# Kernel tuning notes

Measured on AMD Instinct MI355X. Metric: run time of the kernel, lower is better.

The kernel has to match this reference:

```python
import jax, jax.numpy as jnp
import numpy as np

NUM_CLASSES = 80
TOPK = 1000
CONF_THRESH = 0.05
NMS_THRESH = 0.6
IMG = 1280.0  # input image H = W
LEVEL_N = [230400, 57600, 14400, 3600, 900]  # (1280/stride)^2 * 9 anchors, strides 8..128


def _make_boxes(k, n):
    kc, kw = jax.random.split(k)
    cxcy = jax.random.uniform(kc, (n, 2), jnp.float32, 0.0, IMG)
    wh = jax.random.uniform(kw, (n, 2), jnp.float32, 8.0, 256.0)
    x1y1 = jnp.clip(cxcy - 0.5 * wh, 0.0, IMG)
    x2y2 = jnp.clip(cxcy + 0.5 * wh, 0.0, IMG)
    return jnp.concatenate([x1y1, x2y2], axis=-1)  # [n,4] xyxy pixel coords


def setup_inputs() -> dict:
    key = jax.random.key(0)
    keys = jax.random.split(key, 10)
    inp = {}
    for i, n in enumerate(LEVEL_N):
        inp[f"cls{i}"] = jax.random.normal(keys[i], (n, NUM_CLASSES), jnp.float32) - 2.0
        inp[f"box{i}"] = _make_boxes(keys[5 + i], n)
    return inp


def _level_topk(cls_l, box_l):
    # cls_l: [N, C] logits, box_l: [N, 4]
    n = cls_l.shape[0]
    scores = jax.nn.sigmoid(cls_l).reshape(-1)           # [N*C]
    k = min(TOPK, n)
    top_scores, top_idx = jax.lax.top_k(scores, k)       # fused sort/topk per level
    labels = top_idx % NUM_CLASSES
    anchor = top_idx // NUM_CLASSES
    boxes = box_l[anchor]                                # irregular gather
    valid = top_scores > CONF_THRESH
    return top_scores, labels, boxes, valid


def _pairwise_iou(b):
    # b: [M,4] xyxy
    area = jnp.maximum(b[:, 2] - b[:, 0], 0.0) * jnp.maximum(b[:, 3] - b[:, 1], 0.0)
    lt = jnp.maximum(b[:, None, :2], b[None, :, :2])
    rb = jnp.minimum(b[:, None, 2:], b[None, :, 2:])
    wh = jnp.maximum(rb - lt, 0.0)
    inter = wh[..., 0] * wh[..., 1]
    return inter / (area[:, None] + area[None, :] - inter + 1e-9)


def _greedy_nms(boxes, scores, labels, valid):
    # class-aware greedy NMS via per-class coordinate offset trick
    m = scores.shape[0]
    s = jnp.where(valid, scores, 0.0)
    order = jnp.argsort(-s)
    boxes = boxes[order]
    s = s[order]
    labels = labels[order]
    valid = valid[order]
    offset = labels.astype(boxes.dtype)[:, None] * (IMG + 1.0)
    ious = _pairwise_iou(boxes + offset)                 # [M,M]
    idx = jnp.arange(m)

    def body(i, keep):
        sup = keep[i] & (ious[i] > NMS_THRESH) & (idx > i)
        return keep & ~sup

    keep = jax.lax.fori_loop(0, m, body, valid)
    return boxes, s, labels, keep


def reference(cls0, cls1, cls2, cls3, cls4, box0, box1, box2, box3, box4):
    cls_preds = [cls0, cls1, cls2, cls3, cls4]
    box_preds = [box0, box1, box2, box3, box4]
    parts = [_level_topk(c, b) for c, b in zip(cls_preds, box_preds)]
    scores = jnp.concatenate([p[0] for p in parts])
    labels = jnp.concatenate([p[1] for p in parts])
    boxes = jnp.concatenate([p[2] for p in parts])
    valid = jnp.concatenate([p[3] for p in parts])
    boxes, scores, labels, keep = _greedy_nms(boxes, scores, labels, valid)
    keepf = keep.astype(boxes.dtype)
    bboxes = jnp.clip(boxes / IMG, 0.0, 1.0) * keepf[:, None]  # normalize like inference_single_image
    scores = scores * keepf
    return bboxes, scores, labels, keep
```

## Files before the change

kernel.cpp:

```cpp
#include <hip/hip_runtime.h>
#include <cmath>

typedef unsigned int u32;
typedef unsigned long long u64;

#define NLEV 5
#define M_TOT 4900
#define NWORDS 77
#define CSTRIDE 80
#define PAD_M 4928
#define NBLK 1501
#define LDSQ 2048
#define NSH 32
#define SHCAP 2048
#define OVCAP 16384
#define LVST (NSH*SHCAP + OVCAP)
#define TIE_CAP 2048
#define NBLK_CMAT 3003
#define HBINS 4096
#define UCAP 128

__constant__ int   c_KLVL[5] = {1000,1000,1000,1000,900};
__constant__ int   c_LOFF[5] = {0,1000,2000,3000,4000};
__constant__ int   c_N4[5]   = {4608000,1152000,288000,72000,18000};
__constant__ int   c_BB[6]   = {0,1125,1407,1478,1496,1501};
__constant__ float c_THR[5]  = {1.0f,0.65f,0.30f,-0.15f,-0.60f};

constexpr size_t OFF_CNT   = 0;
constexpr size_t OFF_OCNT  = 768;
constexpr size_t OFF_KEPT  = 1024;
constexpr size_t OFF_HPRED = 2048;
constexpr size_t ZERO_BYTES= 4096;
constexpr size_t OFF_CAND  = 4096;
constexpr size_t OFF_KEY   = OFF_CAND + (size_t)NLEV*LVST*8;
constexpr size_t OFF_RAWB  = OFF_KEY   + (size_t)PAD_M*8;
constexpr size_t OFF_OFFB  = OFF_RAWB  + (size_t)PAD_M*16;
constexpr size_t OFF_LAB   = OFF_OFFB  + (size_t)PAD_M*16;
constexpr size_t OFF_SVAL  = OFF_LAB   + (size_t)PAD_M*4;
constexpr size_t OFF_VALID = OFF_SVAL  + (size_t)PAD_M*4;
constexpr size_t OFF_SRAWB = OFF_VALID + (size_t)PAD_M*4;
constexpr size_t OFF_SOFFB = OFF_SRAWB + (size_t)PAD_M*16;
constexpr size_t OFF_SLAB  = OFF_SOFFB + (size_t)PAD_M*16;
constexpr size_t OFF_SSVAL = OFF_SLAB  + (size_t)PAD_M*4;
constexpr size_t OFF_SVALID= OFF_SSVAL + (size_t)PAD_M*4;
constexpr size_t OFF_CMAT  = (OFF_SVALID + (size_t)PAD_M*4 + 255) & ~(size_t)255;

__device__ __forceinline__ u32 okey(u32 u){
  return (u & 0x80000000u) ? ~u : (u | 0x80000000u);
}

__device__ __forceinline__ u32 qbin(u32 bits, float T){
  float x = __uint_as_float(bits);
  int b = (int)((x - T)*800.0f);
  return (u32)max(0, min(HBINS-1, b));
}

__device__ __forceinline__ u32 lane_prior(u64 mask){
  return __builtin_amdgcn_mbcnt_hi((u32)(mask>>32),
         __builtin_amdgcn_mbcnt_lo((u32)mask, 0u));
}

__device__ __forceinline__ u32 wave_alloc(u32* ctr, bool take){
  u64 mask = __ballot(take);
  if (mask==0ull) return 0xFFFFFFFFu;
  u32 prior = lane_prior(mask);
  u32 total = (u32)__popcll(mask);
  int leader = __ffsll((unsigned long long)mask) - 1;
  u32 base = 0;
  if (take && prior==0u) base = atomicAdd(ctr, total);
  base = __shfl(base, leader, 64);
  return take ? (base + prior) : 0xFFFFFFFFu;
}

__global__ void __launch_bounds__(256)
k_collect(const float* __restrict__ a0, const float* __restrict__ a1,
          const float* __restrict__ a2, const float* __restrict__ a3,
          const float* __restrict__ a4,
          u32* __restrict__ cnt, u32* __restrict__ ocnt, u32* __restrict__ cand)
{
  const int b = blockIdx.x;
  const int l = (b<c_BB[1])?0:(b<c_BB[2])?1:(b<c_BB[3])?2:(b<c_BB[4])?3:4;
  const float* __restrict__ p = (l==0)?a0:(l==1)?a1:(l==2)?a2:(l==3)?a3:a4;
  const float T = c_THR[l];
  const int n4l = c_N4[l];
  const int lb  = b - c_BB[l];
  const int shard = lb & (NSH-1);
  const int base4 = lb*4096 + (int)threadIdx.x;

  __shared__ u32 lcnt, gbase;
  __shared__ u32 lbitsA[LDSQ];
  __shared__ u32 lidxA[LDSQ];
  if (threadIdx.x==0) lcnt=0u;
  __syncthreads();

  float4 xs[16];
#pragma unroll
  for (int u=0;u<16;u++){
    int q = base4 + u*256;
    int qc = (q < n4l) ? q : (n4l-1);
    xs[u] = *(const float4*)(p + (size_t)qc*4u);
  }
  u32* cdS = cand + ((size_t)l*LVST + (size_t)shard*SHCAP)*2u;
  u32* cdO = cand + ((size_t)l*LVST + (size_t)NSH*SHCAP)*2u;
#pragma unroll
  for (int u=0;u<16;u++){
    int q = base4 + u*256;
    if (q < n4l){
      float v[4]={xs[u].x,xs[u].y,xs[u].z,xs[u].w};
#pragma unroll
      for (int i=0;i<4;i++){
        if (v[i] > T){
          u32 s = atomicAdd(&lcnt,1u);
          u32 bits = __float_as_uint(v[i]);
          u32 idx  = (u32)(q*4+i);
          if (s < LDSQ){ lbitsA[s]=bits; lidxA[s]=idx; }
          else {
            u32 pp = atomicAdd(&ocnt[l],1u);
            if (pp < OVCAP){ u32* d=cdO+(size_t)pp*2u; d[0]=bits; d[1]=idx; }
          }
        }
      }
    }
  }
  __syncthreads();
  if (threadIdx.x==0){
    u32 m = min(lcnt,(u32)LDSQ);
    gbase = (m>0u) ? atomicAdd(&cnt[l*NSH+shard],m) : 0xFFFFFFFFu;
  }
  __syncthreads();
  u32 m = min(lcnt,(u32)LDSQ);
  for (u32 i=threadIdx.x;i<m;i+=256u){
    u32 pp = gbase + i;
    if (pp < SHCAP){ u32* d=cdS+(size_t)pp*2u; d[0]=lbitsA[i]; d[1]=lidxA[i]; }
    else {
      u32 q = atomicAdd(&ocnt[l],1u);
      if (q < OVCAP){ u32* d=cdO+(size_t)q*2u; d[0]=lbitsA[i]; d[1]=lidxA[i]; }
    }
  }
}

__device__ __forceinline__ void emit_record(int l, int slot, u32 lbits, u32 idx,
    const float4* __restrict__ boxp, u64* keyA, float4* rawbA, float4* offbA,
    u32* labA, float* svalA, u32* validA)
{
#pragma clang fp contract(off)
  float x = __uint_as_float(lbits);
  float s = (float)(1.0 / (1.0 + exp(-(double)x)));
  u32 valid = (s > 0.05f) ? 1u : 0u;
  u32 label = idx % 80u;
  u32 anchor = idx / 80u;
  float4 bx = boxp[anchor];
  float off = (float)label * 1281.0f;
  float4 ob;
  ob.x = bx.x + off; ob.y = bx.y + off; ob.z = bx.z + off; ob.w = bx.w + off;
  u32 pos = ((u32)l << 25) | idx;
  u32 khi = valid ? okey(lbits) : 0u;
  int g = c_LOFF[l] + slot;
  keyA[g]  = ((u64)khi << 32) | (u64)(u32)(~pos);
  rawbA[g] = bx; offbA[g] = ob; labA[g] = label;
  svalA[g] = valid ? s : 0.0f; validA[g] = valid;
}

__device__ __forceinline__ void emit_dummy(int l, int slot,
    u64* keyA, float4* rawbA, float4* offbA, u32* labA, float* svalA, u32* validA)
{
  u32 pos = ((u32)l<<25) | (0x1FFFFFFu - (u32)slot);
  int g = c_LOFF[l]+slot;
  float4 z; z.x=z.y=z.z=z.w=0.0f;
  keyA[g]=(u64)(u32)(~pos);
  rawbA[g]=z; offbA[g]=z; labA[g]=0u; svalA[g]=0.0f; validA[g]=0u;
}

__global__ void __launch_bounds__(1024)
k_select(u32* __restrict__ cnt, u32* __restrict__ ocnt, u32* __restrict__ cand,
         const float* __restrict__ a0, const float* __restrict__ a1,
         const float* __restrict__ a2, const float* __restrict__ a3,
         const float* __restrict__ a4,
         const float4* b0, const float4* b1, const float4* b2,
         const float4* b3, const float4* b4,
         u64* keyA, float4* rawbA, float4* offbA,
         u32* labA, float* svalA, u32* validA)
{
  const int l = blockIdx.x;
  const float4* boxp = (l==0)?b0:(l==1)?b1:(l==2)?b2:(l==3)?b3:b4;
  const float* __restrict__ p = (l==0)?a0:(l==1)?a1:(l==2)?a2:(l==3)?a3:a4;
  const float Tl = c_THR[l];
  u32* lvbase = cand + (size_t)l*LVST*2u;
  u32* cdO = lvbase + (size_t)NSH*SHCAP*2u;
  const int k = c_KLVL[l];

  __shared__ u32 lhist[4][HBINS];
  __shared__ u32 sufw[16];
  __shared__ u32 rlen[NSH+1];
  __shared__ u32 count_s;
  __shared__ u32 c0_s, kk_s;
  __shared__ u32 emit_s, ntie_s;
  __shared__ u32 tb[TIE_CAP], ti[TIE_CAP];

  const u32 tid = threadIdx.x;
  const u32 lane = tid & 63u;
  const u32 wave = tid >> 6;
  if (tid==0){ emit_s=0u; ntie_s=0u; c0_s=0u; kk_s=0u; }
  if (tid<NSH) rlen[tid]=min(cnt[l*NSH+tid],(u32)SHCAP);
  if (tid==NSH) rlen[NSH]=min(ocnt[l],(u32)OVCAP);
  for (u32 i=tid;i<4u*HBINS;i+=1024u) ((u32*)lhist)[i]=0u;
  __syncthreads();
  if (tid==0){ u32 c=0; for(int r=0;r<=NSH;r++) c+=rlen[r]; count_s=c; }
  __syncthreads();
  u32 count = count_s;

  if (count < (u32)k){
    const int nElem = c_N4[l]*4;
    float Tprev = Tl;
    for (int r=1; r<=7 && count<(u32)k; r++){
      float Tn = (r<7) ? (Tl - 1.5f*(float)r) : -3.0e38f;
      for (u32 i=tid; i<(u32)nElem; i+=1024u){
        float x = p[i];
        if (x>Tn && x<=Tprev){
          u32 pp = atomicAdd(&ocnt[l],1u);
          if (pp<OVCAP){ u32* d=cdO+(size_t)pp*2u; d[0]=__float_as_uint(x); d[1]=i; }
        }
      }
      __syncthreads();
      if (tid==0){
        rlen[NSH]=min(atomicAdd(&ocnt[l],0u),(u32)OVCAP);
        u32 c=0; for(int rr=0;rr<=NSH;rr++) c+=rlen[rr]; count_s=c;
      }
      __syncthreads();
      count = count_s;
      Tprev = Tn;
    }
  }

  if (count > (u32)k){
    const u32 rep = wave & 3u;
    for (int r=0;r<=NSH;r++){
      const u32* cdR = lvbase + ((r<NSH)?(size_t)r*SHCAP:(size_t)NSH*SHCAP)*2u;
      u32 len = rlen[r];
      for (u32 i=tid;i<len;i+=1024u)
        atomicAdd(&lhist[rep][qbin(cdR[2*(size_t)i],Tl)], 1u);
    }
    __syncthreads();
    u32 base = tid*4u;
    u32 hb[4]; u32 ls=0u;
#pragma unroll
    for (int b2_=0;b2_<4;b2_++){
      u32 h = lhist[0][base+(u32)b2_]+lhist[1][base+(u32)b2_]
            + lhist[2][base+(u32)b2_]+lhist[3][base+(u32)b2_];
      hb[b2_]=h; ls+=h;
    }
    u32 x = ls;
#pragma unroll
    for (int off=1; off<64; off<<=1){
      u32 y = __shfl_down(x, off, 64);
      if (lane + (u32)off < 64u) x += y;
    }
    if (lane==0u) sufw[wave]=x;
    __syncthreads();
    u32 wsuf=0u;
    for (u32 w=wave+1u;w<16u;w++) wsuf += sufw[w];
    u32 suffix_after = wsuf + (x - ls);
    if (suffix_after < (u32)k && (u32)k <= suffix_after + ls){
      u32 run = suffix_after;
      for (int b2_=3;b2_>=0;b2_--){
        u32 h = hb[b2_];
        run += h;
        if (run >= (u32)k){ c0_s = base+(u32)b2_; kk_s = (u32)k - (run - h); break; }
      }
    }
    __syncthreads();
    const u32 c0 = c0_s, kk = kk_s;

    for (int r=0;r<=NSH;r++){
      const u32* cdR = lvbase + ((r<NSH)?(size_t)r*SHCAP:(size_t)NSH*SHCAP)*2u;
      u32 len = rlen[r];
      u32 iters = (len + 1023u)/1024u;
      for (u32 it=0; it<iters; it++){
        u32 i = it*1024u + tid;
        bool in = i < len;
        u32 bits = in ? cdR[2*(size_t)i] : 0u;
        u32 idx  = in ? cdR[2*(size_t)i+1] : 0u;
        u32 h    = qbin(bits,Tl);
        bool hi  = in && (h > c0);
        bool tie = in && (h == c0);
        u32 s = wave_alloc(&emit_s, hi);
        if (hi && s < (u32)k)
          emit_record(l,(int)s,bits,idx,boxp,keyA,rawbA,offbA,labA,svalA,validA);
        u32 t = wave_alloc(&ntie_s, tie);
        if (tie && t < (u32)TIE_CAP){ tb[t]=bits; ti[t]=idx; }
      }
    }
    __syncthreads();

    u32 nt = ntie_s;
    if (nt <= (u32)TIE_CAP){
      for (u32 e=tid;e<nt;e+=1024u){
        u32 mk = okey(tb[e]); u32 mi = ti[e];
        u32 r=0u;
        for (u32 e2=0;e2<nt;e2++){
          u32 k2 = okey(tb[e2]);
          r += (k2>mk || (k2==mk && ti[e2]<mi)) ? 1u : 0u;
        }
        if (r < kk){
          u32 s = atomicAdd(&emit_s,1u);
          if (s < (u32)k)
            emit_record(l,(int)s,tb[e],mi,boxp,keyA,rawbA,offbA,labA,svalA,validA);
        }
      }
    } else {
      for (int r=0;r<=NSH;r++){
        const u32* cdR = lvbase + ((r<NSH)?(size_t)r*SHCAP:(size_t)NSH*SHCAP)*2u;
        u32 len = rlen[r];
        for (u32 i=tid;i<len;i+=1024u){
          u32 bits=cdR[2*(size_t)i], idx=cdR[2*(size_t)i+1];
          if (qbin(bits,Tl)!=c0) continue;
          u32 mk=okey(bits); u32 rank=0u;
          for (int r2=0;r2<=NSH;r2++){
            const u32* c2 = lvbase + ((r2<NSH)?(size_t)r2*SHCAP:(size_t)NSH*SHCAP)*2u;
            u32 len2 = rlen[r2];
            for (u32 j=0;j<len2;j++){
              u32 b2=c2[2*(size_t)j];
              if (qbin(b2,Tl)!=c0) continue;
              u32 k2=okey(b2);
              rank += (k2>mk || (k2==mk && c2[2*(size_t)j+1]<idx)) ? 1u : 0u;
            }
          }
          if (rank<kk){
            u32 s=atomicAdd(&emit_s,1u);
            if (s<(u32)k)
              emit_record(l,(int)s,bits,idx,boxp,keyA,rawbA,offbA,labA,svalA,validA);
          }
        }
      }
    }
  } else {
    for (int r=0;r<=NSH;r++){
      const u32* cdR = lvbase + ((r<NSH)?(size_t)r*SHCAP:(size_t)NSH*SHCAP)*2u;
      u32 len = rlen[r];
      u32 iters = (len + 1023u)/1024u;
      for (u32 it=0; it<iters; it++){
        u32 i = it*1024u + tid;
        bool in = i < len;
        u32 bits = in ? cdR[2*(size_t)i] : 0u;
        u32 idx  = in ? cdR[2*(size_t)i+1] : 0u;
        u32 s = wave_alloc(&emit_s, in);
        if (in && s < (u32)k)
          emit_record(l,(int)s,bits,idx,boxp,keyA,rawbA,offbA,labA,svalA,validA);
      }
    }
  }
  __syncthreads();
  u32 em = min(emit_s,(u32)k);
  for (u32 i=em+tid;i<(u32)k;i+=1024u)
    emit_dummy(l,(int)i,keyA,rawbA,offbA,labA,svalA,validA);
}

__global__ void __launch_bounds__(256)
k_rank(const u64* __restrict__ keyA,
       const float4* __restrict__ rawbA, const float4* __restrict__ offbA,
       const u32* __restrict__ labA, const float* __restrict__ svalA,
       const u32* __restrict__ validA,
       float4* srawb, float4* soffb, u32* slab, float* ssval, u32* svalid)
{
  __shared__ u64 sk[M_TOT];
  __shared__ u32 part[3][64];
  for (int i=threadIdx.x;i<M_TOT;i+=256) sk[i]=keyA[i];
  __syncthreads();
  int lane = threadIdx.x & 63;
  int wave = threadIdx.x >> 6;
  int i = blockIdx.x*64 + lane;
  u64 mk = sk[(i<M_TOT)?i:0];
  int j0 = wave*1225;
  u32 r=0;
#pragma unroll 5
  for (int j=j0;j<j0+1225;j++) r += (sk[j]>mk)?1u:0u;
  if (wave) part[wave-1][lane]=r;
  __syncthreads();
  if (wave==0 && i<M_TOT){
    r += part[0][lane]+part[1][lane]+part[2][lane];
    srawb[r]=rawbA[i]; soffb[r]=offbA[i]; slab[r]=labA[i];
    ssval[r]=svalA[i]; svalid[r]=validA[i];
  }
}

__global__ void __launch_bounds__(256)
k_cmat(const float4* __restrict__ soffb, u64* __restrict__ cmat,
       u64* __restrict__ haspred)
{
#pragma clang fp contract(off)
  int bi = blockIdx.x;
  int jt = (int)((sqrtf(8.0f*(float)bi+1.0f)-1.0f)*0.5f);
  while ((jt+1)*(jt+2)/2 <= bi) jt++;
  while (jt*(jt+1)/2 > bi) jt--;
  int wt = bi - jt*(jt+1)/2;

  __shared__ float rx[64],ry[64],rz[64],rw[64],ra[64];
  __shared__ float cx[64],cy[64],cz[64],cw[64],cae[64];
  int tid = threadIdx.x;
  if (tid<64){
    float4 b = soffb[wt*64+tid];
    rx[tid]=b.x; ry[tid]=b.y; rz[tid]=b.z; rw[tid]=b.w;
    ra[tid]=fmaxf(b.z-b.x,0.0f)*fmaxf(b.w-b.y,0.0f);
  } else if (tid<128){
    int c=tid-64;
    float4 b = soffb[jt*64+c];
    cx[c]=b.x; cy[c]=b.y; cz[c]=b.z; cw[c]=b.w;
    cae[c]=fmaxf(b.z-b.x,0.0f)*fmaxf(b.w-b.y,0.0f);
  }
  __syncthreads();
  int lane = tid & 63;
  int wave = tid >> 6;
  int rowg = wt*64 + lane;
  float bx=rx[lane], by=ry[lane], bz=rz[lane], bw=rw[lane], bar=ra[lane];
  for (int cc=wave*16; cc<wave*16+16; cc++){
    int jg = jt*64 + cc;
    if (jg >= M_TOT) continue;
    float jx=cx[cc], jy=cy[cc], jz=cz[cc], jw=cw[cc], jar=cae[cc];
    float ltx=fmaxf(bx,jx), lty=fmaxf(by,jy);
    float rbx=fminf(bz,jz), rby=fminf(bw,jw);
    float wx=fmaxf(rbx-ltx,0.0f), wy=fmaxf(rby-lty,0.0f);
    float inter=wx*wy;
    float iou = inter/(bar+jar-inter+1e-9f);
    bool bit = (rowg < jg) && (iou > 0.6f);
    u64 word = __ballot(bit);
    if (lane==0){
      cmat[(size_t)jg*CSTRIDE + (size_t)wt] = word;
      if (word) atomicOr(&haspred[jg>>6], 1ull<<(jg&63));
    }
  }
}

__global__ void __launch_bounds__(256)
k_resolve(const u64* __restrict__ cmat, const u32* __restrict__ svalid,
          const u64* __restrict__ haspred, u64* __restrict__ kept)
{
  __shared__ u64 k0[NWORDS];
  __shared__ u64 uw[NWORDS];
  __shared__ u32 ubase[NWORDS];
  __shared__ unsigned short ulist[UCAP];
  __shared__ u64 pmask[UCAP][2];
  __shared__ u32 dhit[UCAP];
  __shared__ u32 nu_s;
  const u32 tid=threadIdx.x, lane=tid&63u, wave=tid>>6;

  for (u32 w=wave; w<NWORDS; w+=4){
    int j = (int)(w*64u+lane);
    u32 sv = (j<M_TOT)? svalid[j] : 0u;
    u64 hp = haspred[w];
    bool hpb = (hp>>lane)&1ull;
    u64 keepb = __ballot(sv && !hpb);
    u64 undb  = __ballot(sv && hpb);
    if (lane==0){ k0[w]=keepb; uw[w]=undb; }
  }
  __syncthreads();
  if (tid==0){
    u32 n=0;
    for (int w=0;w<NWORDS;w++){
      ubase[w]=n;
      u64 U=uw[w];
      while(U){ int b=__builtin_ctzll(U); U&=U-1ull;
                if (n<UCAP) ulist[n]=(unsigned short)(w*64+b); n++; }
    }
    nu_s=n;
  }
  __syncthreads();
  u32 nu = nu_s;

  if (nu>0u && nu<=UCAP){
    for (u32 t=tid; t<nu; t+=256u){
      u32 j = (u32)ulist[t];
      const u64* row = cmat + (size_t)j*CSTRIDE;
      u32 wmax = j>>6;
      u64 hit=0ull, pm0=0ull, pm1=0ull;
      for (u32 w=0; w<=wmax; w++){
        u64 rw = row[w];
        hit |= rw & k0[w];
        u64 ub = rw & uw[w];
        while(ub){
          int b=__builtin_ctzll(ub); ub&=ub-1ull;
          u32 idx = ubase[w] + (u32)__popcll(uw[w] & ((b==0)?0ull:((1ull<<b)-1ull)));
          if (idx<64u) pm0 |= 1ull<<idx; else pm1 |= 1ull<<(idx-64u);
        }
      }
      dhit[t] = (hit!=0ull)?1u:0u;
      pmask[t][0]=pm0; pmask[t][1]=pm1;
    }
    __syncthreads();
    if (tid==0){
      u64 ku0=0ull, ku1=0ull;
      for (u32 t=0;t<nu;t++){
        bool sup = dhit[t] || ((pmask[t][0]&ku0)|(pmask[t][1]&ku1))!=0ull;
        if (!sup){
          if (t<64u) ku0|=1ull<<t; else ku1|=1ull<<(t-64u);
          u32 j=(u32)ulist[t];
          k0[j>>6] |= 1ull<<(j&63u);
        }
      }
    }
    __syncthreads();
  } else if (nu>UCAP){
    if (tid==0){
      for (int w=0;w<NWORDS;w++){
        u64 U=uw[w];
        while(U){
          int b=__builtin_ctzll(U); U&=U-1ull;
          u32 j=(u32)(w*64+b);
          const u64* row = cmat + (size_t)j*CSTRIDE;
          u64 hit=0ull; u32 wmax=j>>6;
          for (u32 w2=0;w2<=wmax;w2++) hit |= row[w2] & k0[w2];
          if (hit==0ull) k0[j>>6] |= 1ull<<(j&63u);
        }
      }
    }
    __syncthreads();
  }
  for (u32 w=tid; w<NWORDS; w+=256u) kept[w]=k0[w];
}

__global__ void k_out(const u64* __restrict__ kept, const float4* __restrict__ srawb,
                      const float* __restrict__ ssval, const u32* __restrict__ slab,
                      float* __restrict__ out)
{
  int t=blockIdx.x*blockDim.x+threadIdx.x;
  if (t<M_TOT){
    u32 kb=(u32)((kept[t>>6]>>(t&63))&1ull);
    float kf=kb?1.0f:0.0f;
    float4 b=srawb[t];
    out[4*t+0]=fminf(fmaxf(b.x/1280.0f,0.0f),1.0f)*kf;
    out[4*t+1]=fminf(fmaxf(b.y/1280.0f,0.0f),1.0f)*kf;
    out[4*t+2]=fminf(fmaxf(b.z/1280.0f,0.0f),1.0f)*kf;
    out[4*t+3]=fminf(fmaxf(b.w/1280.0f,0.0f),1.0f)*kf;
    out[19600+t]=ssval[t]*kf;
    out[24500+t]=(float)slab[t];
    out[29400+t]=kf;
  }
}

extern "C" void kernel_launch(void* const* d_in, const int* in_sizes, int n_in,
                              void* d_out, int out_size, void* d_ws, size_t ws_size,
                              hipStream_t stream)
{
  const float* cls[5]={nullptr,nullptr,nullptr,nullptr,nullptr};
  const float* box[5]={nullptr,nullptr,nullptr,nullptr,nullptr};
  static const int clsEl[5]={18432000,4608000,1152000,288000,72000};
  static const int boxEl[5]={921600,230400,57600,14400,3600};
  for (int i=0;i<n_in;i++){
    int sz=in_sizes[i];
    bool done=false;
    for (int l=0;l<5 && !done;l++){
      if (sz==clsEl[l] && !cls[l]){ cls[l]=(const float*)d_in[i]; done=true; }
      else if (sz==boxEl[l] && !box[l]){ box[l]=(const float*)d_in[i]; done=true; }
    }
  }
  unsigned char* ws=(unsigned char*)d_ws;
  u32* cnt   = (u32*)(ws+OFF_CNT);
  u32* ocnt  = (u32*)(ws+OFF_OCNT);
  u64* kept  = (u64*)(ws+OFF_KEPT);
  u64* hpred = (u64*)(ws+OFF_HPRED);
  u32* cand  = (u32*)(ws+OFF_CAND);
  u64* keyA  = (u64*)(ws+OFF_KEY);
  float4* rawbA=(float4*)(ws+OFF_RAWB);
  float4* offbA=(float4*)(ws+OFF_OFFB);
  u32* labA  = (u32*)(ws+OFF_LAB);
  float* svalA=(float*)(ws+OFF_SVAL);
  u32* validA=(u32*)(ws+OFF_VALID);
  float4* srawb=(float4*)(ws+OFF_SRAWB);
  float4* soffb=(float4*)(ws+OFF_SOFFB);
  u32* slab  = (u32*)(ws+OFF_SLAB);
  float* ssval=(float*)(ws+OFF_SSVAL);
  u32* svalid=(u32*)(ws+OFF_SVALID);
  u64* cmat  = (u64*)(ws+OFF_CMAT);
  float* out = (float*)d_out;

  hipMemsetAsync(ws, 0, ZERO_BYTES, stream);

  k_collect<<<dim3(NBLK),dim3(256),0,stream>>>(cls[0],cls[1],cls[2],cls[3],cls[4],cnt,ocnt,cand);

  k_select<<<dim3(5),dim3(1024),0,stream>>>(cnt,ocnt,cand,
      cls[0],cls[1],cls[2],cls[3],cls[4],
      (const float4*)box[0],(const float4*)box[1],(const float4*)box[2],
      (const float4*)box[3],(const float4*)box[4],
      keyA,rawbA,offbA,labA,svalA,validA);

  k_rank  <<<dim3(77),dim3(256),0,stream>>>(keyA,rawbA,offbA,labA,svalA,validA,
                                            srawb,soffb,slab,ssval,svalid);
  k_cmat  <<<dim3(NBLK_CMAT),dim3(256),0,stream>>>(soffb,cmat,hpred);
  k_resolve<<<dim3(1),dim3(256),0,stream>>>(cmat,svalid,hpred,kept);
  k_out   <<<dim3(20),dim3(256),0,stream>>>(kept,srawb,ssval,slab,out);
}
```

Measured before the change: 285.4 us.

## Split per-level top-k selection into multi-block histogram, cut, emit and tie kernels

The single-block-per-level selection kernel is replaced by four kernels. A histogram pass runs one block per candidate region and merges into a global per-level histogram. A small kernel finds the cut bin. An emit pass, again one block per region, writes records above the cut and gathers tie-bin candidates into a global buffer. A final per-level kernel ranks the ties and pads with dummy records. The collect kernel also uses twice as many blocks, each processing half as many elements. This spreads the serial selection work over many CUs, at the cost of more kernel launches and extra global atomics and buffers.

Result: faster. 238.7 us (-16.4%).

```diff
diff --git a/kernel.cpp b/kernel.cpp
--- a/kernel.cpp
+++ b/kernel.cpp
@@ -9,13 +9,14 @@
 #define NWORDS 77
 #define CSTRIDE 80
 #define PAD_M 4928
-#define NBLK 1501
+#define NBLK 2999
 #define LDSQ 2048
 #define NSH 32
 #define SHCAP 2048
 #define OVCAP 16384
+#define NREG 33
 #define LVST (NSH*SHCAP + OVCAP)
-#define TIE_CAP 2048
+#define TIE_CAP 4096
 #define NBLK_CMAT 3003
 #define HBINS 4096
 #define UCAP 128
@@ -23,15 +24,21 @@
 __constant__ int   c_KLVL[5] = {1000,1000,1000,1000,900};
 __constant__ int   c_LOFF[5] = {0,1000,2000,3000,4000};
 __constant__ int   c_N4[5]   = {4608000,1152000,288000,72000,18000};
-__constant__ int   c_BB[6]   = {0,1125,1407,1478,1496,1501};
+__constant__ int   c_BB[6]   = {0,2250,2813,2954,2990,2999};
 __constant__ float c_THR[5]  = {1.0f,0.65f,0.30f,-0.15f,-0.60f};
 
 constexpr size_t OFF_CNT   = 0;
 constexpr size_t OFF_OCNT  = 768;
 constexpr size_t OFF_KEPT  = 1024;
 constexpr size_t OFF_HPRED = 2048;
-constexpr size_t ZERO_BYTES= 4096;
-constexpr size_t OFF_CAND  = 4096;
+constexpr size_t OFF_C0    = 2816;
+constexpr size_t OFF_KK    = 2848;
+constexpr size_t OFF_EMITC = 2880;
+constexpr size_t OFF_TIEC  = 2912;
+constexpr size_t OFF_GHIST = 4096;
+constexpr size_t ZERO_BYTES= OFF_GHIST + (size_t)NLEV*HBINS*4;
+constexpr size_t OFF_TIEB  = ZERO_BYTES;
+constexpr size_t OFF_CAND  = OFF_TIEB + (size_t)NLEV*TIE_CAP*8;
 constexpr size_t OFF_KEY   = OFF_CAND + (size_t)NLEV*LVST*8;
 constexpr size_t OFF_RAWB  = OFF_KEY   + (size_t)PAD_M*8;
 constexpr size_t OFF_OFFB  = OFF_RAWB  + (size_t)PAD_M*16;
@@ -72,6 +79,10 @@
   return take ? (base + prior) : 0xFFFFFFFFu;
 }
 
+__device__ __forceinline__ const u32* region_ptr(u32* cand, int l, int r){
+  return cand + ((size_t)l*LVST + ((r<NSH)?(size_t)r*SHCAP:(size_t)NSH*SHCAP))*2u;
+}
+
 __global__ void __launch_bounds__(256)
 k_collect(const float* __restrict__ a0, const float* __restrict__ a1,
           const float* __restrict__ a2, const float* __restrict__ a3,
@@ -85,7 +96,7 @@
   const int n4l = c_N4[l];
   const int lb  = b - c_BB[l];
   const int shard = lb & (NSH-1);
-  const int base4 = lb*4096 + (int)threadIdx.x;
+  const int base4 = lb*2048 + (int)threadIdx.x;
 
   __shared__ u32 lcnt, gbase;
   __shared__ u32 lbitsA[LDSQ];
@@ -93,9 +104,9 @@
   if (threadIdx.x==0) lcnt=0u;
   __syncthreads();
 
-  float4 xs[16];
+  float4 xs[8];
 #pragma unroll
-  for (int u=0;u<16;u++){
+  for (int u=0;u<8;u++){
     int q = base4 + u*256;
     int qc = (q < n4l) ? q : (n4l-1);
     xs[u] = *(const float4*)(p + (size_t)qc*4u);
@@ -103,7 +114,7 @@
   u32* cdS = cand + ((size_t)l*LVST + (size_t)shard*SHCAP)*2u;
   u32* cdO = cand + ((size_t)l*LVST + (size_t)NSH*SHCAP)*2u;
 #pragma unroll
-  for (int u=0;u<16;u++){
+  for (int u=0;u<8;u++){
     int q = base4 + u*256;
     if (q < n4l){
       float v[4]={xs[u].x,xs[u].y,xs[u].z,xs[u].w};
@@ -137,6 +148,112 @@
       if (q < OVCAP){ u32* d=cdO+(size_t)q*2u; d[0]=lbitsA[i]; d[1]=lidxA[i]; }
     }
   }
+}
+
+__global__ void __launch_bounds__(256)
+k_hist(const u32* __restrict__ cnt, const u32* __restrict__ ocnt,
+       u32* __restrict__ cand, u32* __restrict__ ghist)
+{
+  const int l = blockIdx.x / NREG;
+  const int r = blockIdx.x % NREG;
+  const u32 len = (r<NSH) ? min(cnt[l*NSH+r],(u32)SHCAP) : min(ocnt[l],(u32)OVCAP);
+  __shared__ u32 lh[HBINS];
+  for (u32 i=threadIdx.x;i<(u32)HBINS;i+=256u) lh[i]=0u;
+  __syncthreads();
+  if (len){
+    const u32* cdR = region_ptr(cand,l,r);
+    const float Tl = c_THR[l];
+    for (u32 i=threadIdx.x;i<len;i+=256u)
+      atomicAdd(&lh[qbin(cdR[2*(size_t)i],Tl)],1u);
+  }
+  __syncthreads();
+  u32* gh = ghist + (u32)l*HBINS;
+  for (u32 i=threadIdx.x;i<(u32)HBINS;i+=256u){
+    u32 v=lh[i];
+    if (v) atomicAdd(&gh[i],v);
+  }
+}
+
+__global__ void __launch_bounds__(1024)
+k_cut(u32* __restrict__ cnt, u32* __restrict__ ocnt, u32* __restrict__ cand,
+      u32* __restrict__ ghist,
+      const float* __restrict__ a0, const float* __restrict__ a1,
+      const float* __restrict__ a2, const float* __restrict__ a3,
+      const float* __restrict__ a4,
+      u32* __restrict__ c0A, u32* __restrict__ kkA)
+{
+  const int l = blockIdx.x;
+  const int k = c_KLVL[l];
+  const float Tl = c_THR[l];
+  const float* __restrict__ p = (l==0)?a0:(l==1)?a1:(l==2)?a2:(l==3)?a3:a4;
+  u32* cdO = cand + ((size_t)l*LVST + (size_t)NSH*SHCAP)*2u;
+  u32* gh = ghist + (u32)l*HBINS;
+
+  __shared__ u32 rlen[NREG];
+  __shared__ u32 count_s, sufw[16];
+  __shared__ u32 c0_s, kk_s;
+  const u32 tid=threadIdx.x, lane=tid&63u, wave=tid>>6;
+  if (tid<NSH) rlen[tid]=min(cnt[l*NSH+tid],(u32)SHCAP);
+  if (tid==NSH) rlen[NSH]=min(ocnt[l],(u32)OVCAP);
+  if (tid==0){ c0_s=0u; kk_s=(u32)k; }
+  __syncthreads();
+  if (tid==0){ u32 c=0; for(int r=0;r<NREG;r++) c+=rlen[r]; count_s=c; }
+  __syncthreads();
+  u32 count = count_s;
+
+  if (count < (u32)k){
+    const int nElem = c_N4[l]*4;
+    float Tprev = Tl;
+    u32 oc0 = rlen[NSH];
+    for (int r=1; r<=7 && count<(u32)k; r++){
+      float Tn = (r<7) ? (Tl - 1.5f*(float)r) : -3.0e38f;
+      for (u32 i=tid; i<(u32)nElem; i+=1024u){
+        float x = p[i];
+        if (x>Tn && x<=Tprev){
+          u32 pp = atomicAdd(&ocnt[l],1u);
+          if (pp<OVCAP){ u32* d=cdO+(size_t)pp*2u; d[0]=__float_as_uint(x); d[1]=i; }
+        }
+      }
+      __syncthreads();
+      if (tid==0){
+        rlen[NSH]=min(atomicAdd(&ocnt[l],0u),(u32)OVCAP);
+        u32 c=0; for(int rr=0;rr<NREG;rr++) c+=rlen[rr]; count_s=c;
+      }
+      __syncthreads();
+      count = count_s;
+      Tprev = Tn;
+    }
+    if (tid==0 && rlen[NSH]>oc0) atomicAdd(&gh[0], rlen[NSH]-oc0);
+    __syncthreads();
+  }
+
+  if (count > (u32)k){
+    u32 base = tid*4u;
+    u32 hb[4]; u32 ls=0u;
+#pragma unroll
+    for (int b2_=0;b2_<4;b2_++){ u32 h=gh[base+(u32)b2_]; hb[b2_]=h; ls+=h; }
+    u32 x = ls;
+#pragma unroll
+    for (int off=1; off<64; off<<=1){
+      u32 y = __shfl_down(x, off, 64);
+      if (lane + (u32)off < 64u) x += y;
+    }
+    if (lane==0u) sufw[wave]=x;
+    __syncthreads();
+    u32 wsuf=0u;
+    for (u32 w=wave+1u;w<16u;w++) wsuf += sufw[w];
+    u32 suffix_after = wsuf + (x - ls);
+    if (suffix_after < (u32)k && (u32)k <= suffix_after + ls){
+      u32 run = suffix_after;
+      for (int b2_=3;b2_>=0;b2_--){
+        u32 h = hb[b2_];
+        run += h;
+        if (run >= (u32)k){ c0_s = base+(u32)b2_; kk_s = (u32)k - (run - h); break; }
+      }
+    }
+    __syncthreads();
+  }
+  if (tid==0){ c0A[l]=c0_s; kkA[l]=kk_s; }
 }
 
 __device__ __forceinline__ void emit_record(int l, int slot, u32 lbits, u32 idx,
@@ -171,186 +288,141 @@
   rawbA[g]=z; offbA[g]=z; labA[g]=0u; svalA[g]=0.0f; validA[g]=0u;
 }
 
+__global__ void __launch_bounds__(256)
+k_emit(const u32* __restrict__ cnt, const u32* __restrict__ ocnt,
+       u32* __restrict__ cand,
+       const u32* __restrict__ c0A,
+       u32* __restrict__ emitc, u32* __restrict__ tiec, u32* __restrict__ tieb,
+       const float4* b0, const float4* b1, const float4* b2,
+       const float4* b3, const float4* b4,
+       u64* keyA, float4* rawbA, float4* offbA,
+       u32* labA, float* svalA, u32* validA)
+{
+  const int l = blockIdx.x / NREG;
+  const int r = blockIdx.x % NREG;
+  const u32 len = (r<NSH) ? min(cnt[l*NSH+r],(u32)SHCAP) : min(ocnt[l],(u32)OVCAP);
+  if (len==0u) return;
+  const float4* boxp = (l==0)?b0:(l==1)?b1:(l==2)?b2:(l==3)?b3:b4;
+  const u32* cdR = region_ptr(cand,l,r);
+  const float Tl = c_THR[l];
+  const u32 c0 = c0A[l];
+  const int k = c_KLVL[l];
+  u32* tbL = tieb + (size_t)l*TIE_CAP*2u;
+
+  __shared__ u32 wb[1024], wi[1024], tb2[1024], ti2[1024];
+  __shared__ u32 nw_s, nt_s, gb_s, tgb_s;
+  const u32 tid=threadIdx.x;
+  if (tid==0){ nw_s=0u; nt_s=0u; }
+  __syncthreads();
+
+  u32 iters=(len+255u)/256u;
+  for (u32 it=0; it<iters; it++){
+    u32 i = it*256u + tid;
+    bool in = i < len;
+    u32 bits = in ? cdR[2*(size_t)i] : 0u;
+    u32 idx  = in ? cdR[2*(size_t)i+1] : 0u;
+    u32 h    = in ? qbin(bits,Tl) : 0u;
+    bool hi  = in && (h > c0);
+    bool tie = in && (h == c0);
+    u32 s = wave_alloc(&nw_s, hi);
+    if (hi && s<1024u){ wb[s]=bits; wi[s]=idx; }
+    u32 t = wave_alloc(&nt_s, tie);
+    if (tie){
+      if (t<1024u){ tb2[t]=bits; ti2[t]=idx; }
+      else {
+        u32 g=atomicAdd(&tiec[l],1u);
+        if (g<(u32)TIE_CAP){ tbL[2u*g]=bits; tbL[2u*g+1u]=idx; }
+      }
+    }
+  }
+  __syncthreads();
+  u32 nw = min(nw_s,1024u), nt = min(nt_s,1024u);
+  if (tid==0){
+    gb_s  = nw ? atomicAdd(&emitc[l], nw) : 0u;
+    tgb_s = nt ? atomicAdd(&tiec[l], nt) : 0u;
+  }
+  __syncthreads();
+  for (u32 i=tid;i<nw;i+=256u){
+    u32 slot = gb_s + i;
+    if ((int)slot < k)
+      emit_record(l,(int)slot,wb[i],wi[i],boxp,keyA,rawbA,offbA,labA,svalA,validA);
+  }
+  for (u32 i=tid;i<nt;i+=256u){
+    u32 g = tgb_s + i;
+    if (g<(u32)TIE_CAP){ tbL[2u*g]=tb2[i]; tbL[2u*g+1u]=ti2[i]; }
+  }
+}
+
 __global__ void __launch_bounds__(1024)
-k_select(u32* __restrict__ cnt, u32* __restrict__ ocnt, u32* __restrict__ cand,
-         const float* __restrict__ a0, const float* __restrict__ a1,
-         const float* __restrict__ a2, const float* __restrict__ a3,
-         const float* __restrict__ a4,
-         const float4* b0, const float4* b1, const float4* b2,
-         const float4* b3, const float4* b4,
-         u64* keyA, float4* rawbA, float4* offbA,
-         u32* labA, float* svalA, u32* validA)
+k_tie(const u32* __restrict__ cnt, const u32* __restrict__ ocnt,
+      u32* __restrict__ cand,
+      const u32* __restrict__ c0A, const u32* __restrict__ kkA,
+      u32* __restrict__ emitc, const u32* __restrict__ tiec,
+      const u32* __restrict__ tieb,
+      const float4* b0, const float4* b1, const float4* b2,
+      const float4* b3, const float4* b4,
+      u64* keyA, float4* rawbA, float4* offbA,
+      u32* labA, float* svalA, u32* validA)
 {
   const int l = blockIdx.x;
   const float4* boxp = (l==0)?b0:(l==1)?b1:(l==2)?b2:(l==3)?b3:b4;
-  const float* __restrict__ p = (l==0)?a0:(l==1)?a1:(l==2)?a2:(l==3)?a3:a4;
+  const int k = c_KLVL[l];
+  const u32 kk = kkA[l];
+  const u32 c0 = c0A[l];
   const float Tl = c_THR[l];
-  u32* lvbase = cand + (size_t)l*LVST*2u;
-  u32* cdO = lvbase + (size_t)NSH*SHCAP*2u;
-  const int k = c_KLVL[l];
-
-  __shared__ u32 lhist[4][HBINS];
-  __shared__ u32 sufw[16];
-  __shared__ u32 rlen[NSH+1];
-  __shared__ u32 count_s;
-  __shared__ u32 c0_s, kk_s;
-  __shared__ u32 emit_s, ntie_s;
+  const u32* tbL = tieb + (size_t)l*TIE_CAP*2u;
+  const u32 ntg = tiec[l];
+  const u32 tid = threadIdx.x;
+
   __shared__ u32 tb[TIE_CAP], ti[TIE_CAP];
 
-  const u32 tid = threadIdx.x;
-  const u32 lane = tid & 63u;
-  const u32 wave = tid >> 6;
-  if (tid==0){ emit_s=0u; ntie_s=0u; c0_s=0u; kk_s=0u; }
-  if (tid<NSH) rlen[tid]=min(cnt[l*NSH+tid],(u32)SHCAP);
-  if (tid==NSH) rlen[NSH]=min(ocnt[l],(u32)OVCAP);
-  for (u32 i=tid;i<4u*HBINS;i+=1024u) ((u32*)lhist)[i]=0u;
-  __syncthreads();
-  if (tid==0){ u32 c=0; for(int r=0;r<=NSH;r++) c+=rlen[r]; count_s=c; }
-  __syncthreads();
-  u32 count = count_s;
-
-  if (count < (u32)k){
-    const int nElem = c_N4[l]*4;
-    float Tprev = Tl;
-    for (int r=1; r<=7 && count<(u32)k; r++){
-      float Tn = (r<7) ? (Tl - 1.5f*(float)r) : -3.0e38f;
-      for (u32 i=tid; i<(u32)nElem; i+=1024u){
-        float x = p[i];
-        if (x>Tn && x<=Tprev){
-          u32 pp = atomicAdd(&ocnt[l],1u);
-          if (pp<OVCAP){ u32* d=cdO+(size_t)pp*2u; d[0]=__float_as_uint(x); d[1]=i; }
-        }
-      }
-      __syncthreads();
-      if (tid==0){
-        rlen[NSH]=min(atomicAdd(&ocnt[l],0u),(u32)OVCAP);
-        u32 c=0; for(int rr=0;rr<=NSH;rr++) c+=rlen[rr]; count_s=c;
-      }
-      __syncthreads();
-      count = count_s;
-      Tprev = Tn;
-    }
-  }
-
-  if (count > (u32)k){
-    const u32 rep = wave & 3u;
-    for (int r=0;r<=NSH;r++){
-      const u32* cdR = lvbase + ((r<NSH)?(size_t)r*SHCAP:(size_t)NSH*SHCAP)*2u;
-      u32 len = rlen[r];
-      for (u32 i=tid;i<len;i+=1024u)
-        atomicAdd(&lhist[rep][qbin(cdR[2*(size_t)i],Tl)], 1u);
-    }
+  if (ntg <= (u32)TIE_CAP){
+    for (u32 i=tid;i<ntg;i+=1024u){ tb[i]=tbL[2u*i]; ti[i]=tbL[2u*i+1u]; }
     __syncthreads();
-    u32 base = tid*4u;
-    u32 hb[4]; u32 ls=0u;
-#pragma unroll
-    for (int b2_=0;b2_<4;b2_++){
-      u32 h = lhist[0][base+(u32)b2_]+lhist[1][base+(u32)b2_]
-            + lhist[2][base+(u32)b2_]+lhist[3][base+(u32)b2_];
-      hb[b2_]=h; ls+=h;
-    }
-    u32 x = ls;
-#pragma unroll
-    for (int off=1; off<64; off<<=1){
-      u32 y = __shfl_down(x, off, 64);
-      if (lane + (u32)off < 64u) x += y;
-    }
-    if (lane==0u) sufw[wave]=x;
-    __syncthreads();
-    u32 wsuf=0u;
-    for (u32 w=wave+1u;w<16u;w++) wsuf += sufw[w];
-    u32 suffix_after = wsuf + (x - ls);
-    if (suffix_after < (u32)k && (u32)k <= suffix_after + ls){
-      u32 run = suffix_after;
-      for (int b2_=3;b2_>=0;b2_--){
-        u32 h = hb[b2_];
-        run += h;
-        if (run >= (u32)k){ c0_s = base+(u32)b2_; kk_s = (u32)k - (run - h); break; }
-      }
-    }
-    __syncthreads();
-    const u32 c0 = c0_s, kk = kk_s;
-
-    for (int r=0;r<=NSH;r++){
-      const u32* cdR = lvbase + ((r<NSH)?(size_t)r*SHCAP:(size_t)NSH*SHCAP)*2u;
-      u32 len = rlen[r];
-      u32 iters = (len + 1023u)/1024u;
-      for (u32 it=0; it<iters; it++){
-        u32 i = it*1024u + tid;
-        bool in = i < len;
-        u32 bits = in ? cdR[2*(size_t)i] : 0u;
-        u32 idx  = in ? cdR[2*(size_t)i+1] : 0u;
-        u32 h    = qbin(bits,Tl);
-        bool hi  = in && (h > c0);
-        bool tie = in && (h == c0);
-        u32 s = wave_alloc(&emit_s, hi);
-        if (hi && s < (u32)k)
-          emit_record(l,(int)s,bits,idx,boxp,keyA,rawbA,offbA,labA,svalA,validA);
-        u32 t = wave_alloc(&ntie_s, tie);
-        if (tie && t < (u32)TIE_CAP){ tb[t]=bits; ti[t]=idx; }
-      }
-    }
-    __syncthreads();
-
-    u32 nt = ntie_s;
-    if (nt <= (u32)TIE_CAP){
-      for (u32 e=tid;e<nt;e+=1024u){
-        u32 mk = okey(tb[e]); u32 mi = ti[e];
-        u32 r=0u;
-        for (u32 e2=0;e2<nt;e2++){
-          u32 k2 = okey(tb[e2]);
-          r += (k2>mk || (k2==mk && ti[e2]<mi)) ? 1u : 0u;
-        }
-        if (r < kk){
-          u32 s = atomicAdd(&emit_s,1u);
-          if (s < (u32)k)
-            emit_record(l,(int)s,tb[e],mi,boxp,keyA,rawbA,offbA,labA,svalA,validA);
-        }
-      }
-    } else {
-      for (int r=0;r<=NSH;r++){
-        const u32* cdR = lvbase + ((r<NSH)?(size_t)r*SHCAP:(size_t)NSH*SHCAP)*2u;
-        u32 len = rlen[r];
-        for (u32 i=tid;i<len;i+=1024u){
-          u32 bits=cdR[2*(size_t)i], idx=cdR[2*(size_t)i+1];
-          if (qbin(bits,Tl)!=c0) continue;
-          u32 mk=okey(bits); u32 rank=0u;
-          for (int r2=0;r2<=NSH;r2++){
-            const u32* c2 = lvbase + ((r2<NSH)?(size_t)r2*SHCAP:(size_t)NSH*SHCAP)*2u;
-            u32 len2 = rlen[r2];
-            for (u32 j=0;j<len2;j++){
-              u32 b2=c2[2*(size_t)j];
-              if (qbin(b2,Tl)!=c0) continue;
-              u32 k2=okey(b2);
-              rank += (k2>mk || (k2==mk && c2[2*(size_t)j+1]<idx)) ? 1u : 0u;
-            }
-          }
-          if (rank<kk){
-            u32 s=atomicAdd(&emit_s,1u);
-            if (s<(u32)k)
-              emit_record(l,(int)s,bits,idx,boxp,keyA,rawbA,offbA,labA,svalA,validA);
+    for (u32 e=tid;e<ntg;e+=1024u){
+      u32 mk = okey(tb[e]); u32 mi = ti[e];
+      u32 r=0u;
+      for (u32 e2=0;e2<ntg;e2++){
+        u32 k2 = okey(tb[e2]);
+        r += (k2>mk || (k2==mk && ti[e2]<mi)) ? 1u : 0u;
+      }
+      if (r < kk){
+        u32 s = atomicAdd(&emitc[l],1u);
+        if ((int)s < k)
+          emit_record(l,(int)s,tb[e],mi,boxp,keyA,rawbA,offbA,labA,svalA,validA);
+      }
+    }
+  } else {
+    for (int r0=0;r0<NREG;r0++){
+      const u32* cdR = region_ptr(cand,l,r0);
+      u32 len = (r0<NSH)?min(cnt[l*NSH+r0],(u32)SHCAP):min(ocnt[l],(u32)OVCAP);
+      for (u32 i=tid;i<len;i+=1024u){
+        u32 bits=cdR[2*(size_t)i], idx=cdR[2*(size_t)i+1];
+        if (qbin(bits,Tl)!=c0) continue;
+        u32 mk=okey(bits); u32 rank=0u;
+        for (int r2=0;r2<NREG;r2++){
+          const u32* c2 = region_ptr(cand,l,r2);
+          u32 len2 = (r2<NSH)?min(cnt[l*NSH+r2],(u32)SHCAP):min(ocnt[l],(u32)OVCAP);
+          for (u32 j=0;j<len2;j++){
+            u32 b2=c2[2*(size_t)j];
+            if (qbin(b2,Tl)!=c0) continue;
+            u32 k2=okey(b2);
+            rank += (k2>mk || (k2==mk && c2[2*(size_t)j+1]<idx)) ? 1u : 0u;
           }
         }
-      }
-    }
-  } else {
-    for (int r=0;r<=NSH;r++){
-      const u32* cdR = lvbase + ((r<NSH)?(size_t)r*SHCAP:(size_t)NSH*SHCAP)*2u;
-      u32 len = rlen[r];
-      u32 iters = (len + 1023u)/1024u;
-      for (u32 it=0; it<iters; it++){
-        u32 i = it*1024u + tid;
-        bool in = i < len;
-        u32 bits = in ? cdR[2*(size_t)i] : 0u;
-        u32 idx  = in ? cdR[2*(size_t)i+1] : 0u;
-        u32 s = wave_alloc(&emit_s, in);
-        if (in && s < (u32)k)
-          emit_record(l,(int)s,bits,idx,boxp,keyA,rawbA,offbA,labA,svalA,validA);
-      }
-    }
-  }
-  __syncthreads();
-  u32 em = min(emit_s,(u32)k);
+        if (rank<kk){
+          u32 s=atomicAdd(&emitc[l],1u);
+          if ((int)s<k)
+            emit_record(l,(int)s,bits,idx,boxp,keyA,rawbA,offbA,labA,svalA,validA);
+        }
+      }
+    }
+  }
+  __syncthreads();
+  __shared__ u32 em_s;
+  if (tid==0) em_s = atomicAdd(&emitc[l],0u);
+  __syncthreads();
+  u32 em = min(em_s,(u32)k);
   for (u32 i=em+tid;i<(u32)k;i+=1024u)
     emit_dummy(l,(int)i,keyA,rawbA,offbA,labA,svalA,validA);
 }
@@ -557,6 +629,12 @@
   u32* ocnt  = (u32*)(ws+OFF_OCNT);
   u64* kept  = (u64*)(ws+OFF_KEPT);
   u64* hpred = (u64*)(ws+OFF_HPRED);
+  u32* c0A   = (u32*)(ws+OFF_C0);
+  u32* kkA   = (u32*)(ws+OFF_KK);
+  u32* emitc = (u32*)(ws+OFF_EMITC);
+  u32* tiec  = (u32*)(ws+OFF_TIEC);
+  u32* ghist = (u32*)(ws+OFF_GHIST);
+  u32* tieb  = (u32*)(ws+OFF_TIEB);
   u32* cand  = (u32*)(ws+OFF_CAND);
   u64* keyA  = (u64*)(ws+OFF_KEY);
   float4* rawbA=(float4*)(ws+OFF_RAWB);
@@ -575,16 +653,20 @@
   hipMemsetAsync(ws, 0, ZERO_BYTES, stream);
 
   k_collect<<<dim3(NBLK),dim3(256),0,stream>>>(cls[0],cls[1],cls[2],cls[3],cls[4],cnt,ocnt,cand);
-
-  k_select<<<dim3(5),dim3(1024),0,stream>>>(cnt,ocnt,cand,
-      cls[0],cls[1],cls[2],cls[3],cls[4],
-      (const float4*)box[0],(const float4*)box[1],(const float4*)box[2],
-      (const float4*)box[3],(const float4*)box[4],
-      keyA,rawbA,offbA,labA,svalA,validA);
-
-  k_rank  <<<dim3(77),dim3(256),0,stream>>>(keyA,rawbA,offbA,labA,svalA,validA,
-                                            srawb,soffb,slab,ssval,svalid);
-  k_cmat  <<<dim3(NBLK_CMAT),dim3(256),0,stream>>>(soffb,cmat,hpred);
+  k_hist   <<<dim3(NLEV*NREG),dim3(256),0,stream>>>(cnt,ocnt,cand,ghist);
+  k_cut    <<<dim3(NLEV),dim3(1024),0,stream>>>(cnt,ocnt,cand,ghist,
+              cls[0],cls[1],cls[2],cls[3],cls[4],c0A,kkA);
+  k_emit   <<<dim3(NLEV*NREG),dim3(256),0,stream>>>(cnt,ocnt,cand,c0A,emitc,tiec,tieb,
+              (const float4*)box[0],(const float4*)box[1],(const float4*)box[2],
+              (const float4*)box[3],(const float4*)box[4],
+              keyA,rawbA,offbA,labA,svalA,validA);
+  k_tie    <<<dim3(NLEV),dim3(1024),0,stream>>>(cnt,ocnt,cand,c0A,kkA,emitc,tiec,tieb,
+              (const float4*)box[0],(const float4*)box[1],(const float4*)box[2],
+              (const float4*)box[3],(const float4*)box[4],
+              keyA,rawbA,offbA,labA,svalA,validA);
+  k_rank   <<<dim3(77),dim3(256),0,stream>>>(keyA,rawbA,offbA,labA,svalA,validA,
+                                             srawb,soffb,slab,ssval,svalid);
+  k_cmat   <<<dim3(NBLK_CMAT),dim3(256),0,stream>>>(soffb,cmat,hpred);
   k_resolve<<<dim3(1),dim3(256),0,stream>>>(cmat,svalid,hpred,kept);
-  k_out   <<<dim3(20),dim3(256),0,stream>>>(kept,srawb,ssval,slab,out);
-}
+  k_out    <<<dim3(20),dim3(256),0,stream>>>(kept,srawb,ssval,slab,out);
+}
```
